# Optimization experiments

Hardware: AMD Instinct MI355X
Metric: run time of the kernel (lower is better)

The kernel has to match this reference:

```python
import jax, jax.numpy as jnp
import numpy as np
import math

HIDDEN = 256
NUM_HEADS = 8
HEAD_DIM = HIDDEN // NUM_HEADS  # 32
SCALE = math.sqrt(HEAD_DIM)
B, N, E = 1, 20000, 320000


def setup_inputs() -> dict:
    key = jax.random.key(0)
    kq, kk, kv, ke = jax.random.split(key, 4)
    q = jax.random.normal(kq, (B, N, HIDDEN), dtype=jnp.float32)
    k = jax.random.normal(kk, (B, N, HIDDEN), dtype=jnp.float32)
    v = jax.random.normal(kv, (B, N, HIDDEN), dtype=jnp.float32)
    edge_index = jax.random.randint(ke, (2, E), 0, N, dtype=jnp.int64)
    return {"q": q, "k": k, "v": v, "edge_index": edge_index}


def reference(q, k, v, edge_index):
    batch_size, node_num = q.shape[0], q.shape[1]
    # flatten batch*node axis, split heads: [B*N, H, D]
    qf = q.reshape(-1, NUM_HEADS, HEAD_DIM)
    kf = k.reshape(-1, NUM_HEADS, HEAD_DIM)
    vf = v.reshape(-1, NUM_HEADS, HEAD_DIM)
    src_idx = edge_index[0]
    dst_idx = edge_index[1]
    src = kf[src_idx]    # [E, H, D] gathered keys
    dest = qf[dst_idx]   # [E, H, D] gathered queries
    # unnormalized exp score per edge/head, clamped like the torch code
    score = jnp.clip(jnp.sum(src * dest, axis=-1, keepdims=True) / SCALE, -5.0, 5.0)
    score = jnp.exp(score)                 # [E, H, 1]
    msg = vf[src_idx] * score              # [E, H, D]
    num_seg = qf.shape[0]
    wV = jax.ops.segment_sum(msg, dst_idx, num_segments=num_seg)    # [B*N, H, D]
    Z = jax.ops.segment_sum(score, dst_idx, num_segments=num_seg)   # [B*N, H, 1]
    x = wV / (Z + 1e-6)
    return x.reshape(batch_size, node_num, -1)
```

## Files before the change

### kernel.cpp

```cpp
#include <hip/hip_runtime.h>
#include <hip/hip_fp16.h>
#include <math.h>

#define NHEADS 8
#define HIDDEN 256
#define F4_PER_ROW 64
#define INV_SCALE 0.17677669529663687f
#define ELL_W 64

#define SCAN_THREADS 1024
#define SCAN_CHUNK 20


union H4 { float2 f; __half2 h[2]; };

__global__ void __launch_bounds__(256)
build_kernel(const float4* __restrict__ kf4, const float4* __restrict__ vf4,
             float2* __restrict__ k16, float2* __restrict__ v16,
             const int* __restrict__ src, const int* __restrict__ dst,
             int* __restrict__ cnt, int* __restrict__ ell,
             int nf4, int E) {
    int stride = gridDim.x * blockDim.x;
    int tid0 = blockIdx.x * blockDim.x + threadIdx.x;

    for (int i = tid0; i < nf4; i += stride) {
        float4 x = kf4[i];
        H4 u;
        u.h[0] = __floats2half2_rn(x.x, x.y);
        u.h[1] = __floats2half2_rn(x.z, x.w);
        k16[i] = u.f;
        float4 y = vf4[i];
        H4 w;
        w.h[0] = __floats2half2_rn(y.x, y.y);
        w.h[1] = __floats2half2_rn(y.z, y.w);
        v16[i] = w.f;
    }

    int nq = E >> 2;
    for (int q = tid0; q < nq; q += stride) {
        int4 s = ((const int4*)src)[q];
        int4 d = ((const int4*)dst)[q];
        int sl;
        sl = atomicAdd(&cnt[d.x], 1); if (sl < ELL_W) ell[d.x * ELL_W + sl] = s.x;
        sl = atomicAdd(&cnt[d.y], 1); if (sl < ELL_W) ell[d.y * ELL_W + sl] = s.y;
        sl = atomicAdd(&cnt[d.z], 1); if (sl < ELL_W) ell[d.z * ELL_W + sl] = s.z;
        sl = atomicAdd(&cnt[d.w], 1); if (sl < ELL_W) ell[d.w * ELL_W + sl] = s.w;
    }
    if (tid0 == 0) {
        for (int i = (E >> 2) << 2; i < E; ++i) {
            int t = dst[i];
            int sl = atomicAdd(&cnt[t], 1);
            if (sl < ELL_W) ell[t * ELL_W + sl] = src[i];
        }
    }
}

__device__ __forceinline__ float dot4h(float2 pk, float4 q) {
    H4 u; u.f = pk;
    float2 a = __half22float2(u.h[0]);
    float2 b = __half22float2(u.h[1]);
    return a.x * q.x + a.y * q.y + b.x * q.z + b.y * q.w;
}

__device__ __forceinline__ void acc4h(float2 pv, float sc, float4& acc) {
    H4 u; u.f = pv;
    float2 a = __half22float2(u.h[0]);
    float2 b = __half22float2(u.h[1]);
    acc.x += a.x * sc; acc.y += a.y * sc;
    acc.z += b.x * sc; acc.w += b.y * sc;
}

__device__ __forceinline__ float hred8(float p) {
    #pragma unroll
    for (int m = 1; m < 8; m <<= 1) p += __shfl_xor(p, m, 8);
    return p;
}

__global__ void __launch_bounds__(256)
gather16_kernel(const float4* __restrict__ q4, const float2* __restrict__ k16,
                const float2* __restrict__ v16, const int* __restrict__ cnt,
                const int* __restrict__ ell, float4* __restrict__ out4, int N) {
    int wid  = threadIdx.x >> 6;
    int lane = threadIdx.x & 63;
    int t = blockIdx.x * 4 + wid;
    if (t >= N) return;

    int deg = cnt[t];
    deg = deg < ELL_W ? deg : ELL_W;
    const int* lst = ell + (long)t * ELL_W;

    long trow = (long)t * F4_PER_ROW;
    float4 qv = q4[trow + lane];

    float4 acc = make_float4(0.f, 0.f, 0.f, 0.f);
    float z = 0.f;

    int i = 0;
    for (; i + 4 <= deg; i += 4) {
        int s0 = lst[i + 0], s1 = lst[i + 1], s2 = lst[i + 2], s3 = lst[i + 3];
        long r0 = (long)s0 * F4_PER_ROW + lane;
        long r1 = (long)s1 * F4_PER_ROW + lane;
        long r2 = (long)s2 * F4_PER_ROW + lane;
        long r3 = (long)s3 * F4_PER_ROW + lane;
        float2 ka = k16[r0], kb = k16[r1], kc = k16[r2], kd = k16[r3];
        float2 va = v16[r0], vb = v16[r1], vc = v16[r2], vd = v16[r3];

        float p0 = hred8(dot4h(ka, qv));
        float p1 = hred8(dot4h(kb, qv));
        float p2 = hred8(dot4h(kc, qv));
        float p3 = hred8(dot4h(kd, qv));

        float sc0 = __expf(fminf(fmaxf(p0 * INV_SCALE, -5.f), 5.f));
        float sc1 = __expf(fminf(fmaxf(p1 * INV_SCALE, -5.f), 5.f));
        float sc2 = __expf(fminf(fmaxf(p2 * INV_SCALE, -5.f), 5.f));
        float sc3 = __expf(fminf(fmaxf(p3 * INV_SCALE, -5.f), 5.f));

        acc4h(va, sc0, acc); acc4h(vb, sc1, acc);
        acc4h(vc, sc2, acc); acc4h(vd, sc3, acc);
        z += sc0 + sc1 + sc2 + sc3;
    }
    for (; i < deg; ++i) {
        int s = lst[i];
        long r = (long)s * F4_PER_ROW + lane;
        float2 kk = k16[r];
        float2 vv = v16[r];
        float p = hred8(dot4h(kk, qv));
        float sc = __expf(fminf(fmaxf(p * INV_SCALE, -5.f), 5.f));
        acc4h(vv, sc, acc);
        z += sc;
    }

    float inv = 1.f / (z + 1e-6f);
    float4 o;
    o.x = acc.x * inv; o.y = acc.y * inv; o.z = acc.z * inv; o.w = acc.w * inv;
    out4[trow + lane] = o;
}


__global__ void __launch_bounds__(256)
histogram_kernel(const int* __restrict__ dst, int* __restrict__ cnt, int E) {
    int i = (blockIdx.x * blockDim.x + threadIdx.x) * 4;
    if (i + 3 < E) {
        int4 d = *(const int4*)(dst + i);
        atomicAdd(&cnt[d.x], 1);
        atomicAdd(&cnt[d.y], 1);
        atomicAdd(&cnt[d.z], 1);
        atomicAdd(&cnt[d.w], 1);
    } else {
        for (; i < E; ++i) atomicAdd(&cnt[dst[i]], 1);
    }
}

__global__ void __launch_bounds__(SCAN_THREADS)
scan_kernel(const int* __restrict__ cnt, int* __restrict__ off, int N) {
    __shared__ int wsum[16];
    __shared__ int wpre[16];
    int t = threadIdx.x;
    int lane = t & 63;
    int wv = t >> 6;
    int base = t * SCAN_CHUNK;
    int local[SCAN_CHUNK];
    int sum = 0;
    #pragma unroll
    for (int j = 0; j < SCAN_CHUNK; ++j) {
        int i = base + j;
        int c = (i < N) ? cnt[i] : 0;
        local[j] = c;
        sum += c;
    }
    int x = sum;
    #pragma unroll
    for (int d = 1; d < 64; d <<= 1) {
        int y = __shfl_up(x, d, 64);
        if (lane >= d) x += y;
    }
    if (lane == 63) wsum[wv] = x;
    __syncthreads();
    if (t < 16) {
        int v = wsum[t];
        #pragma unroll
        for (int d = 1; d < 16; d <<= 1) {
            int y = __shfl_up(v, d, 16);
            if (t >= d) v += y;
        }
        wpre[t] = v;
    }
    __syncthreads();
    int run = (wv ? wpre[wv - 1] : 0) + (x - sum);
    #pragma unroll
    for (int j = 0; j < SCAN_CHUNK; ++j) {
        int i = base + j;
        if (i <= N) off[i] = run;
        run += local[j];
    }
}

__global__ void __launch_bounds__(256)
scatter_kernel(const int* __restrict__ src, const int* __restrict__ dst,
               const int* __restrict__ off, int* __restrict__ cnt,
               int* __restrict__ csr_src, int E) {
    int i = (blockIdx.x * blockDim.x + threadIdx.x) * 4;
    if (i + 3 < E) {
        int4 s = *(const int4*)(src + i);
        int4 d = *(const int4*)(dst + i);
        csr_src[off[d.x] + atomicSub(&cnt[d.x], 1) - 1] = s.x;
        csr_src[off[d.y] + atomicSub(&cnt[d.y], 1) - 1] = s.y;
        csr_src[off[d.z] + atomicSub(&cnt[d.z], 1) - 1] = s.z;
        csr_src[off[d.w] + atomicSub(&cnt[d.w], 1) - 1] = s.w;
    } else {
        for (; i < E; ++i) {
            int t = dst[i];
            csr_src[off[t] + atomicSub(&cnt[t], 1) - 1] = src[i];
        }
    }
}

__device__ __forceinline__ float dot4(float4 a, float4 b) {
    return a.x * b.x + a.y * b.y + a.z * b.z + a.w * b.w;
}

__global__ void __launch_bounds__(256)
gather_kernel(const float4* __restrict__ q4, const float4* __restrict__ k4,
              const float4* __restrict__ v4, const int* __restrict__ csr_src,
              const int* __restrict__ off, float4* __restrict__ out4, int N) {
    int wid  = threadIdx.x >> 6;
    int lane = threadIdx.x & 63;
    int t = blockIdx.x * 4 + wid;
    if (t >= N) return;

    int beg = off[t], end = off[t + 1];
    long trow = (long)t * F4_PER_ROW;
    float4 qv = q4[trow + lane];

    float4 acc = make_float4(0.f, 0.f, 0.f, 0.f);
    float z = 0.f;

    for (int i = beg; i < end; ++i) {
        int s = csr_src[i];
        long r = (long)s * F4_PER_ROW + lane;
        float4 kv = k4[r];
        float4 vv = v4[r];
        float p = hred8(dot4(kv, qv));
        float sc = __expf(fminf(fmaxf(p * INV_SCALE, -5.f), 5.f));
        acc.x += vv.x * sc;
        acc.y += vv.y * sc;
        acc.z += vv.z * sc;
        acc.w += vv.w * sc;
        z += sc;
    }

    float inv = 1.f / (z + 1e-6f);
    float4 o;
    o.x = acc.x * inv; o.y = acc.y * inv; o.z = acc.z * inv; o.w = acc.w * inv;
    out4[trow + lane] = o;
}


extern "C" void kernel_launch(void* const* d_in, const int* in_sizes, int n_in,
                              void* d_out, int out_size, void* d_ws, size_t ws_size,
                              hipStream_t stream) {
    const float* qf = (const float*)d_in[0];
    const float* kf = (const float*)d_in[1];
    const float* vf = (const float*)d_in[2];
    const int*   ei = (const int*)d_in[3];

    int E = in_sizes[3] / 2;
    int N = in_sizes[0] / HIDDEN;
    int nf4 = in_sizes[0] / 4;

    const int* src = ei;
    const int* dst = ei + E;

    size_t need = (size_t)N * 512 * 2 + (size_t)N * ELL_W * 4 + (size_t)N * 4 + 256;

    if (ws_size >= need) {
        char* p = (char*)d_ws;
        float2* k16 = (float2*)p;            p += (size_t)N * 512;
        float2* v16 = (float2*)p;            p += (size_t)N * 512;
        int*    ell = (int*)p;               p += (size_t)N * ELL_W * 4;
        int*    cnt = (int*)p;

        hipMemsetAsync(cnt, 0, (size_t)N * sizeof(int), stream);
        build_kernel<<<2048, 256, 0, stream>>>(
            (const float4*)kf, (const float4*)vf, k16, v16,
            src, dst, cnt, ell, nf4, E);
        gather16_kernel<<<(N + 3) / 4, 256, 0, stream>>>(
            (const float4*)qf, k16, v16, cnt, ell, (float4*)d_out, N);
    } else {
        int* cnt = (int*)d_ws;
        int* off = cnt + N;
        int* csr = off + N + 1;

        hipMemsetAsync(cnt, 0, (size_t)N * sizeof(int), stream);
        int eb = (E / 4 + 255) / 256 + 1;
        histogram_kernel<<<eb, 256, 0, stream>>>(dst, cnt, E);
        scan_kernel<<<1, SCAN_THREADS, 0, stream>>>(cnt, off, N);
        scatter_kernel<<<eb, 256, 0, stream>>>(src, dst, off, cnt, csr, E);
        gather_kernel<<<(N + 3) / 4, 256, 0, stream>>>(
            (const float4*)qf, (const float4*)kf, (const float4*)vf,
            csr, off, (float4*)d_out, N);
    }
}
```

Measured before the change: 161.8 us.

## Interleave fp16 K and V rows into one 1KB record per node for gather

The build kernel now writes each node's fp16 key and value into one contiguous 1KB record, keys in the first half and values in the second. In the gather kernel, lanes 0-31 each load 16 bytes of key (8 halfs) and lanes 32-63 load the matching value bytes, so one 16-byte load per lane per edge replaces two 8-byte loads. Scores are reduced over 4 lanes and broadcast to the value lanes by shuffle, and only the upper half-wave writes output. The build grid is also doubled. The cost is extra cross-lane shuffles and half the wave idle on output stores.

```diff
diff --git a/kernel.cpp b/kernel.cpp
--- a/kernel.cpp
+++ b/kernel.cpp
@@ -13,10 +13,11 @@
 
 
 union H4 { float2 f; __half2 h[2]; };
+union KV8 { float4 f4; __half2 h2[4]; };
 
 __global__ void __launch_bounds__(256)
 build_kernel(const float4* __restrict__ kf4, const float4* __restrict__ vf4,
-             float2* __restrict__ k16, float2* __restrict__ v16,
+             char* __restrict__ kv,
              const int* __restrict__ src, const int* __restrict__ dst,
              int* __restrict__ cnt, int* __restrict__ ell,
              int nf4, int E) {
@@ -24,16 +25,19 @@
     int tid0 = blockIdx.x * blockDim.x + threadIdx.x;
 
     for (int i = tid0; i < nf4; i += stride) {
+        int n = i >> 6;
+        int c = i & 63;
+        char* base = kv + (size_t)n * 1024 + (size_t)c * 8;
         float4 x = kf4[i];
         H4 u;
         u.h[0] = __floats2half2_rn(x.x, x.y);
         u.h[1] = __floats2half2_rn(x.z, x.w);
-        k16[i] = u.f;
+        *(float2*)base = u.f;
         float4 y = vf4[i];
         H4 w;
         w.h[0] = __floats2half2_rn(y.x, y.y);
         w.h[1] = __floats2half2_rn(y.z, y.w);
-        v16[i] = w.f;
+        *(float2*)(base + 512) = w.f;
     }
 
     int nq = E >> 2;
@@ -55,31 +59,33 @@
     }
 }
 
-__device__ __forceinline__ float dot4h(float2 pk, float4 q) {
-    H4 u; u.f = pk;
-    float2 a = __half22float2(u.h[0]);
-    float2 b = __half22float2(u.h[1]);
-    return a.x * q.x + a.y * q.y + b.x * q.z + b.y * q.w;
-}
-
-__device__ __forceinline__ void acc4h(float2 pv, float sc, float4& acc) {
-    H4 u; u.f = pv;
-    float2 a = __half22float2(u.h[0]);
-    float2 b = __half22float2(u.h[1]);
-    acc.x += a.x * sc; acc.y += a.y * sc;
-    acc.z += b.x * sc; acc.w += b.y * sc;
-}
-
-__device__ __forceinline__ float hred8(float p) {
-    #pragma unroll
-    for (int m = 1; m < 8; m <<= 1) p += __shfl_xor(p, m, 8);
-    return p;
-}
-
-__global__ void __launch_bounds__(256)
-gather16_kernel(const float4* __restrict__ q4, const float2* __restrict__ k16,
-                const float2* __restrict__ v16, const int* __restrict__ cnt,
-                const int* __restrict__ ell, float4* __restrict__ out4, int N) {
+__device__ __forceinline__ float edge_score(const KV8& u, float4 qa, float4 qb) {
+    float2 p0 = __half22float2(u.h2[0]);
+    float2 p1 = __half22float2(u.h2[1]);
+    float2 p2 = __half22float2(u.h2[2]);
+    float2 p3 = __half22float2(u.h2[3]);
+    float r = p0.x * qa.x + p0.y * qa.y + p1.x * qa.z + p1.y * qa.w
+            + p2.x * qb.x + p2.y * qb.y + p3.x * qb.z + p3.y * qb.w;
+    r += __shfl_xor(r, 1, 4);
+    r += __shfl_xor(r, 2, 4);
+    return __expf(fminf(fmaxf(r * INV_SCALE, -5.f), 5.f));
+}
+
+__device__ __forceinline__ void acc8(const KV8& u, float sc, float* acc) {
+    float2 w0 = __half22float2(u.h2[0]);
+    float2 w1 = __half22float2(u.h2[1]);
+    float2 w2 = __half22float2(u.h2[2]);
+    float2 w3 = __half22float2(u.h2[3]);
+    acc[0] += w0.x * sc; acc[1] += w0.y * sc;
+    acc[2] += w1.x * sc; acc[3] += w1.y * sc;
+    acc[4] += w2.x * sc; acc[5] += w2.y * sc;
+    acc[6] += w3.x * sc; acc[7] += w3.y * sc;
+}
+
+__global__ void __launch_bounds__(256)
+gather16_kernel(const float4* __restrict__ q4, const char* __restrict__ kv,
+                const int* __restrict__ cnt, const int* __restrict__ ell,
+                float4* __restrict__ out4, int N) {
     int wid  = threadIdx.x >> 6;
     int lane = threadIdx.x & 63;
     int t = blockIdx.x * 4 + wid;
@@ -87,53 +93,62 @@
 
     int deg = cnt[t];
     deg = deg < ELL_W ? deg : ELL_W;
-    const int* lst = ell + (long)t * ELL_W;
+    const int* lst = ell + (size_t)t * ELL_W;
 
     long trow = (long)t * F4_PER_ROW;
-    float4 qv = q4[trow + lane];
-
-    float4 acc = make_float4(0.f, 0.f, 0.f, 0.f);
+    int lk = lane & 31;
+    float4 qa = q4[trow + 2 * lk];
+    float4 qb = q4[trow + 2 * lk + 1];
+    int srcLane = lk & ~3;
+
+    float acc[8] = {0.f, 0.f, 0.f, 0.f, 0.f, 0.f, 0.f, 0.f};
     float z = 0.f;
+    size_t lo = (size_t)lane * 16;
 
     int i = 0;
     for (; i + 4 <= deg; i += 4) {
-        int s0 = lst[i + 0], s1 = lst[i + 1], s2 = lst[i + 2], s3 = lst[i + 3];
-        long r0 = (long)s0 * F4_PER_ROW + lane;
-        long r1 = (long)s1 * F4_PER_ROW + lane;
-        long r2 = (long)s2 * F4_PER_ROW + lane;
-        long r3 = (long)s3 * F4_PER_ROW + lane;
-        float2 ka = k16[r0], kb = k16[r1], kc = k16[r2], kd = k16[r3];
-        float2 va = v16[r0], vb = v16[r1], vc = v16[r2], vd = v16[r3];
-
-        float p0 = hred8(dot4h(ka, qv));
-        float p1 = hred8(dot4h(kb, qv));
-        float p2 = hred8(dot4h(kc, qv));
-        float p3 = hred8(dot4h(kd, qv));
-
-        float sc0 = __expf(fminf(fmaxf(p0 * INV_SCALE, -5.f), 5.f));
-        float sc1 = __expf(fminf(fmaxf(p1 * INV_SCALE, -5.f), 5.f));
-        float sc2 = __expf(fminf(fmaxf(p2 * INV_SCALE, -5.f), 5.f));
-        float sc3 = __expf(fminf(fmaxf(p3 * INV_SCALE, -5.f), 5.f));
-
-        acc4h(va, sc0, acc); acc4h(vb, sc1, acc);
-        acc4h(vc, sc2, acc); acc4h(vd, sc3, acc);
-        z += sc0 + sc1 + sc2 + sc3;
+        int4 ss = *(const int4*)(lst + i);
+        KV8 u0, u1, u2, u3;
+        u0.f4 = *(const float4*)(kv + (size_t)ss.x * 1024 + lo);
+        u1.f4 = *(const float4*)(kv + (size_t)ss.y * 1024 + lo);
+        u2.f4 = *(const float4*)(kv + (size_t)ss.z * 1024 + lo);
+        u3.f4 = *(const float4*)(kv + (size_t)ss.w * 1024 + lo);
+
+        float s0 = edge_score(u0, qa, qb);
+        float s1 = edge_score(u1, qa, qb);
+        float s2 = edge_score(u2, qa, qb);
+        float s3 = edge_score(u3, qa, qb);
+        z += s0 + s1 + s2 + s3;
+
+        float b0 = __shfl(s0, srcLane, 64);
+        float b1 = __shfl(s1, srcLane, 64);
+        float b2 = __shfl(s2, srcLane, 64);
+        float b3 = __shfl(s3, srcLane, 64);
+
+        acc8(u0, b0, acc);
+        acc8(u1, b1, acc);
+        acc8(u2, b2, acc);
+        acc8(u3, b3, acc);
     }
     for (; i < deg; ++i) {
         int s = lst[i];
-        long r = (long)s * F4_PER_ROW + lane;
-        float2 kk = k16[r];
-        float2 vv = v16[r];
-        float p = hred8(dot4h(kk, qv));
-        float sc = __expf(fminf(fmaxf(p * INV_SCALE, -5.f), 5.f));
-        acc4h(vv, sc, acc);
+        KV8 u;
+        u.f4 = *(const float4*)(kv + (size_t)s * 1024 + lo);
+        float sc = edge_score(u, qa, qb);
         z += sc;
-    }
-
-    float inv = 1.f / (z + 1e-6f);
-    float4 o;
-    o.x = acc.x * inv; o.y = acc.y * inv; o.z = acc.z * inv; o.w = acc.w * inv;
-    out4[trow + lane] = o;
+        float b = __shfl(sc, srcLane, 64);
+        acc8(u, b, acc);
+    }
+
+    float zf = __shfl(z, srcLane, 64);
+    float inv = 1.f / (zf + 1e-6f);
+    if (lane >= 32) {
+        int j = lane - 32;
+        float4 o1 = make_float4(acc[0] * inv, acc[1] * inv, acc[2] * inv, acc[3] * inv);
+        float4 o2 = make_float4(acc[4] * inv, acc[5] * inv, acc[6] * inv, acc[7] * inv);
+        out4[trow + 2 * j]     = o1;
+        out4[trow + 2 * j + 1] = o2;
+    }
 }
 
 
@@ -219,6 +234,12 @@
     return a.x * b.x + a.y * b.y + a.z * b.z + a.w * b.w;
 }
 
+__device__ __forceinline__ float hred8(float p) {
+    #pragma unroll
+    for (int m = 1; m < 8; m <<= 1) p += __shfl_xor(p, m, 8);
+    return p;
+}
+
 __global__ void __launch_bounds__(256)
 gather_kernel(const float4* __restrict__ q4, const float4* __restrict__ k4,
               const float4* __restrict__ v4, const int* __restrict__ csr_src,
@@ -271,21 +292,20 @@
     const int* src = ei;
     const int* dst = ei + E;
 
-    size_t need = (size_t)N * 512 * 2 + (size_t)N * ELL_W * 4 + (size_t)N * 4 + 256;
+    size_t need = (size_t)N * 1024 + (size_t)N * ELL_W * 4 + (size_t)N * 4 + 256;
 
     if (ws_size >= need) {
         char* p = (char*)d_ws;
-        float2* k16 = (float2*)p;            p += (size_t)N * 512;
-        float2* v16 = (float2*)p;            p += (size_t)N * 512;
-        int*    ell = (int*)p;               p += (size_t)N * ELL_W * 4;
-        int*    cnt = (int*)p;
+        char* kv  = p;                       p += (size_t)N * 1024;
+        int*  ell = (int*)p;                 p += (size_t)N * ELL_W * 4;
+        int*  cnt = (int*)p;
 
         hipMemsetAsync(cnt, 0, (size_t)N * sizeof(int), stream);
-        build_kernel<<<2048, 256, 0, stream>>>(
-            (const float4*)kf, (const float4*)vf, k16, v16,
+        build_kernel<<<4096, 256, 0, stream>>>(
+            (const float4*)kf, (const float4*)vf, kv,
             src, dst, cnt, ell, nf4, E);
         gather16_kernel<<<(N + 3) / 4, 256, 0, stream>>>(
-            (const float4*)qf, k16, v16, cnt, ell, (float4*)d_out, N);
+            (const float4*)qf, kv, cnt, ell, (float4*)d_out, N);
     } else {
         int* cnt = (int*)d_ws;
         int* off = cnt + N;
```

After: 160.2 us. About the same (-1.0%).
